# Performance work log

Hardware: AMD Instinct MI355X
Metric: run time of the kernel (lower is better)

The kernel has to match this reference:

```python
import jax, jax.numpy as jnp
import numpy as np

G1, G2, G3 = 4.0, 5.0, 10.0   # cfg.SMOOTH.GAMMA1/2/3 (DAMSM defaults)
T_MOCO = 0.05
EPS = 1e-8


def _ce(logits, labels):
    # mean cross-entropy, labels are int class indices
    lp = jax.nn.log_softmax(logits, axis=-1)
    return -jnp.mean(jnp.take_along_axis(lp, labels[:, None], axis=1)[:, 0])


def _norm(x):
    return jnp.sqrt(jnp.sum(x * x, axis=-1, keepdims=True))


def setup_inputs() -> dict:
    key = jax.random.key(0)
    ks = jax.random.split(key, 8)
    B, T, NEF, H, K = 64, 32, 256, 17, 16384
    return {
        "cnn_code": jax.random.normal(ks[0], (B, NEF), jnp.float32),
        "rnn_code": jax.random.normal(ks[1], (B, NEF), jnp.float32),
        "img_features": jax.random.normal(ks[2], (B, NEF, H, H), jnp.float32),
        "words_emb": jax.random.normal(ks[3], (B, T, NEF), jnp.float32),
        "cnn_code_aug": jax.random.normal(ks[4], (B, NEF), jnp.float32),
        "rnn_code_aug": jax.random.normal(ks[5], (B, NEF), jnp.float32),
        "queue": jax.random.normal(ks[6], (NEF, K), jnp.float32),
        "queue_im": jax.random.normal(ks[7], (NEF, K), jnp.float32),
        "sentence_mask": jnp.ones((B, T), jnp.int32),
        "labels": jnp.arange(B, dtype=jnp.int32),
    }


def reference(cnn_code, rnn_code, img_features, words_emb, cnn_code_aug,
              rnn_code_aug, queue, queue_im, sentence_mask, labels):
    B = words_emb.shape[0]
    # ---------- local word-region attention loss (vectorized over the
    # per-sample python loop; sentence_mask is all-ones -> full length) ----------
    q = jnp.transpose(words_emb, (0, 2, 1))                   # [B, nef, T]
    ctx = img_features.reshape(B, img_features.shape[1], -1)  # [B, nef, S]
    # func_attention: scores[i,j,s,t] between query sample i and image j
    scores = jnp.einsum('jcs,ict->ijst', ctx, q)
    attn = jax.nn.softmax(scores, axis=3)        # softmax over words (queryL)
    attn = jax.nn.softmax(G1 * attn, axis=2)     # softmax over regions (sourceL)
    wC = jnp.einsum('jcs,ijst->ijct', ctx, attn)  # weighted context [i,j,nef,T]
    num = jnp.einsum('ict,ijct->ijt', q, wC)
    qn = jnp.sqrt(jnp.sum(q * q, axis=1))[:, None, :]         # [B,1,T]
    wn = jnp.sqrt(jnp.sum(wC * wC, axis=2))                   # [B,B,T]
    cos = num / jnp.clip(qn * wn, EPS, None)                  # [i,j,T]
    sim = jax.nn.logsumexp(G2 * cos, axis=2)                  # log(sum exp(G2*cos))
    S = sim.T * G3                                            # [j, i] as in original cat(dim=1)
    w_loss0 = _ce(S, labels)
    w_loss1 = _ce(S.T, labels)
    # ---------- global contrastive loss ----------
    cn = cnn_code / jnp.clip(_norm(cnn_code), EPS, None)
    rn = rnn_code / jnp.clip(_norm(rnn_code), EPS, None)
    can = cnn_code_aug / jnp.clip(_norm(cnn_code_aug), EPS, None)
    ran = rnn_code_aug / jnp.clip(_norm(rnn_code_aug), EPS, None)
    qz = jax.lax.stop_gradient(queue)
    qzi = jax.lax.stop_gradient(queue_im)
    zeros = jnp.zeros((B,), dtype=labels.dtype)
    log_it = jnp.concatenate([jnp.sum(cn * ran, -1, keepdims=True), cn @ qz], -1) / T_MOCO
    log_ti = jnp.concatenate([jnp.sum(rn * can, -1, keepdims=True), rn @ qzi], -1) / T_MOCO
    m_loss = (_ce(log_it, zeros) + _ce(log_ti, zeros)) / 2.0
    s0 = G3 * (cn @ rn.T)    # cosine(cnn, rnn) * GAMMA3
    s2 = G3 * (rn @ ran.T)   # cosine(rnn, rnn_aug) * GAMMA3
    loss0 = _ce(s0, labels)
    loss1 = _ce(s0.T, labels)
    loss2 = _ce(s2, labels)
    loss3 = _ce(s2.T, labels)
    return jnp.stack([w_loss0, w_loss1, loss0, loss1, m_loss, loss2, loss3])
```

## Files before the change

### kernel.cpp

```cpp
#include <hip/hip_runtime.h>
#include <hip/hip_bf16.h>
#include <math.h>

#define BB   64
#define TT   32
#define CC   256
#define KK   16384
#define G1c  4.0f
#define G2c  5.0f
#define G3c  10.0f
#define INV_T 20.0f
#define EPSF 1e-8f

#define WS_SIM 0
#define WS_S0  4096
#define WS_S2  8192
#define WS_CN  12288
#define WS_RN  28672
#define WS_CAN 45056
#define WS_RAN 61440
#define WS_QN  77824
#define WS_PM  79872
#define WS_PS  (WS_PM + 16384)
#define WS_CNT  (WS_PS + 16384)
#define WS_RNT  (WS_CNT + 16384)
#define WS_CANT (WS_RNT + 16384)
#define WS_RANT (WS_CANT + 16384)
#define WS_F32_TOTAL (WS_RANT + 16384)

#define CTXT_ELEMS (64*320*256)
#define WQ_ELEMS   (64*32*256)
#define WQ_OFF     CTXT_ELEMS
#define CNRN_OFF   (CTXT_ELEMS + WQ_ELEMS)

typedef __attribute__((ext_vector_type(8))) short short8;
typedef __attribute__((ext_vector_type(4))) short short4v;
typedef __attribute__((ext_vector_type(4))) float float4v;

__device__ __forceinline__ float4v mfma_bf16(short8 a, short8 b, float4v c) {
    return __builtin_amdgcn_mfma_f32_16x16x32_bf16(a, b, c, 0, 0, 0);
}

__device__ __forceinline__ short f2bf(float f) {
    union { float f; unsigned u; } x; x.f = f;
    unsigned r = x.u + 0x7FFFu + ((x.u >> 16) & 1u);
    return (short)(r >> 16);
}

__device__ __forceinline__ int swz13(int L) {
    return L ^ (((L>>10)&3)<<4) ^ ((((L>>6)&1) ^ ((L>>10)&1))<<3);
}

__device__ __forceinline__ void stage_tile(const short* g, short* l) {
    #pragma unroll
    for (int m = 0; m < 4; m++)
        __builtin_amdgcn_global_load_lds(
            (const __attribute__((address_space(1))) unsigned int*)(g + m*512),
            (__attribute__((address_space(3))) unsigned int*)(l + m*512),
            16, 0, 0);
}

__global__ __launch_bounds__(256) void prep_kernel(
    const float* __restrict__ cnn, const float* __restrict__ rnn,
    const float* __restrict__ img, const float* __restrict__ wemb,
    const float* __restrict__ cnnA, const float* __restrict__ rnnA,
    float* __restrict__ W)
{
    int bid = blockIdx.x, tid = threadIdx.x;
    short* B16 = (short*)(W + WS_F32_TOTAL);
    short* ctxT = B16;
    short* wq   = B16 + WQ_OFF;
    short* cnrn = B16 + CNRN_OFF;

    if (bid < 256) {
        int mat = bid >> 6, row = bid & 63;
        const float* src = (mat==0)? cnn : (mat==1)? rnn : (mat==2)? cnnA : rnnA;
        float* dst  = W + ((mat==0)? WS_CN  : (mat==1)? WS_RN  : (mat==2)? WS_CAN  : WS_RAN);
        float* dstT = W + ((mat==0)? WS_CNT : (mat==1)? WS_RNT : (mat==2)? WS_CANT : WS_RANT);
        float v = src[row*256 + tid];
        float ss = v*v;
        for (int o=1;o<64;o<<=1) ss += __shfl_xor(ss,o);
        __shared__ float sc[4];
        if ((tid&63)==0) sc[tid>>6] = ss;
        __syncthreads();
        float tot = sc[0]+sc[1]+sc[2]+sc[3];
        float inv = 1.0f / fmaxf(sqrtf(tot), EPSF);
        float nv = v*inv;
        dst[row*256+tid] = nv;
        dstT[tid*64+row] = nv;
        if (mat < 2) cnrn[(mat*64+row)*256 + tid] = f2bf(nv);
    } else if (bid < 320) {
        int i = bid - 256;
        int t = tid >> 3, k = tid & 7;
        const float* wp = wemb + (i*32 + t)*256 + k*32;
        float ss = 0.f;
        for (int c=0;c<32;c++){ float v = wp[c]; ss += v*v; }
        ss += __shfl_xor(ss,1); ss += __shfl_xor(ss,2); ss += __shfl_xor(ss,4);
        if (k==0) W[WS_QN + i*32 + t] = sqrtf(ss);
    } else if (bid < 1600) {
        int b3 = bid - 320; int j = b3 / 20, mt20 = b3 % 20;
        int half = mt20 & 1;
        int s0 = mt20 * 16;
        __shared__ float tbuf[16*257];
        for (int idx = tid; idx < 4096; idx += 256) {
            int c = idx >> 4, sl = idx & 15, s = s0 + sl;
            float v = (s < 289) ? img[((size_t)(j*256 + c))*289 + s] : 0.0f;
            tbuf[sl*257 + c] = v;
        }
        __syncthreads();
        short* dst = ctxT + (size_t)j*81920 + (size_t)mt20*4096;
        for (int idx4 = tid; idx4 < 1024; idx4 += 256) {
            int v = half*4096 + idx4*4;
            int L = swz13(v);
            int sl = ((L>>10)&3)*4 + ((L>>4)&3);
            int c  = ((L>>6)&15)*16 + (L&15);
            const float* tb = &tbuf[sl*257 + c];
            short4v o = { f2bf(tb[0]), f2bf(tb[1]), f2bf(tb[2]), f2bf(tb[3]) };
            *(short4v*)(dst + idx4*4) = o;
        }
    } else {
        for (int idx = (bid-1600)*256 + tid; idx < WQ_ELEMS; idx += 64*256) {
            wq[idx] = f2bf(wemb[idx]);
        }
    }
}

__global__ __launch_bounds__(256, 2) void attn_moco_kernel(
    const float* __restrict__ queue, const float* __restrict__ queueIm,
    float* __restrict__ W)
{
    __shared__ __align__(16) short ctx_sc[2][8192];
    __shared__ __align__(16) short eTile[2][2][32][40];
    __shared__ float Dp[4][32], Np[4][32];
    __shared__ float wn2P[4][2][2][16];
    __shared__ float redm[4][64], reds[4][64];
    __shared__ float sa0[256], sa1[256];
    __shared__ float part[2][64][4];

    int bid = blockIdx.x, tid = threadIdx.x;
    int lane = tid & 63, wave = tid >> 6;
    int lo16 = lane & 15, quad = lane >> 4;

    const short* B16 = (const short*)(W + WS_F32_TOTAL);

    if (bid >= 320) {
        const short* ctxT = B16;
        const short* wq   = B16 + WQ_OFF;

        int abid = bid - 320;
        int j = abid >> 5, ip = abid & 31;
        int i_l = wave >> 1, mt = wave & 1;
        int i_g = ip*2 + i_l;

        short8 bq[2][8];
        {
            const short* p = wq + i_g*8192;
            #pragma unroll
            for (int nt2=0;nt2<2;nt2++)
                #pragma unroll
                for (int kk=0;kk<8;kk++)
                    bq[nt2][kk] = *(const short8*)(p + (nt2*16+lo16)*256 + kk*32 + quad*8);
        }

        float4v wacc[4][4];
        #pragma unroll
        for (int cm=0;cm<4;cm++)
            #pragma unroll
            for (int cb=0;cb<4;cb++) wacc[cm][cb] = (float4v){0.f,0.f,0.f,0.f};
        float D8[8], N8[8];
        #pragma unroll
        for (int u=0;u<8;u++){ D8[u]=0.f; N8[u]=0.f; }

        const short* ctxTj = ctxT + (size_t)j * 81920;

        int s4p = lo16 >> 2;
        int qh = quad >> 1, ql = quad & 1;
        int Lb = (mt*4 + s4p)*1024 + qh*64
               + (((lo16&3) ^ s4p) << 4)
               + ((ql ^ qh ^ (s4p&1)) << 3);
        int pcol = mt*16 + (lo16 & 12) + ((lo16 & 3) ^ s4p);
        unsigned trbase = (unsigned)(unsigned long long)(const void*)(&ctx_sc[0][0])
                        + (unsigned)(quad*4096 + wave*512 + lo16*2);

        stage_tile(ctxTj + 0*8192 + wave*2048 + lane*8, &ctx_sc[0][wave*2048]);
        stage_tile(ctxTj + 1*8192 + wave*2048 + lane*8, &ctx_sc[1][wave*2048]);
        __syncthreads();

        for (int tile = 0; tile < 10; tile++) {
            int cur = tile & 1;
            const short* score_base = &ctx_sc[cur][0] + Lb;

            float4v a0 = {0.f,0.f,0.f,0.f}, a1 = {0.f,0.f,0.f,0.f};
            #pragma unroll
            for (int kk=0;kk<8;kk++) {
                short8 cf = *(const short8*)(score_base + kk*128);
                a0 = mfma_bf16(bq[0][kk], cf, a0);
                a1 = mfma_bf16(bq[1][kk], cf, a1);
            }

            unsigned trA = trbase + (unsigned)(cur*16384);
            unsigned trB = trA ^ 16u;
            short4v w00,w01,w10,w11,w20,w21,w30,w31;
            asm volatile("ds_read_b64_tr_b16 %0, %1 offset:0"    : "=v"(w00) : "v"(trA));
            asm volatile("ds_read_b64_tr_b16 %0, %1 offset:2048" : "=v"(w01) : "v"(trB));
            asm volatile("ds_read_b64_tr_b16 %0, %1 offset:128"  : "=v"(w10) : "v"(trB));
            asm volatile("ds_read_b64_tr_b16 %0, %1 offset:2176" : "=v"(w11) : "v"(trA));
            asm volatile("ds_read_b64_tr_b16 %0, %1 offset:256"  : "=v"(w20) : "v"(trA));
            asm volatile("ds_read_b64_tr_b16 %0, %1 offset:2304" : "=v"(w21) : "v"(trB));
            asm volatile("ds_read_b64_tr_b16 %0, %1 offset:384"  : "=v"(w30) : "v"(trB));
            asm volatile("ds_read_b64_tr_b16 %0, %1 offset:2432" : "=v"(w31) : "v"(trA));

            float mx = fmaxf(fmaxf(fmaxf(a0[0],a0[1]), fmaxf(a0[2],a0[3])),
                             fmaxf(fmaxf(a1[0],a1[1]), fmaxf(a1[2],a1[3])));
            mx = fmaxf(mx, __shfl_xor(mx,16));
            mx = fmaxf(mx, __shfl_xor(mx,32));
            float e0[4], e1[4]; float z = 0.f;
            #pragma unroll
            for (int r=0;r<4;r++) {
                e0[r] = __expf(a0[r]-mx); e1[r] = __expf(a1[r]-mx);
                z += e0[r] + e1[r];
            }
            z += __shfl_xor(z,16); z += __shfl_xor(z,32);
            float grinv = G1c / z;
            int sg = tile*32 + mt*16 + lo16;
            short* et = &eTile[cur][i_l][0][0];
            #pragma unroll
            for (int r=0;r<4;r++) {
                float ev0 = __expf(e0[r]*grinv);
                float ev1 = __expf(e1[r]*grinv);
                if (sg < 289) {
                    D8[r]   += ev0; N8[r]   += ev0*a0[r];
                    D8[4+r] += ev1; N8[4+r] += ev1*a1[r];
                }
                et[(quad*4+r)*40 + pcol]    = f2bf(ev0);
                et[(16+quad*4+r)*40 + pcol] = f2bf(ev1);
            }
            __syncthreads();
            __builtin_amdgcn_sched_barrier(0);
            if (tile < 8)
                stage_tile(ctxTj + (tile+2)*8192 + wave*2048 + lane*8,
                           &ctx_sc[cur][wave*2048]);

            short8 wa_[4];
            wa_[0] = (short8){w00[0],w00[1],w00[2],w00[3], w01[0],w01[1],w01[2],w01[3]};
            wa_[1] = (short8){w10[0],w10[1],w10[2],w10[3], w11[0],w11[1],w11[2],w11[3]};
            wa_[2] = (short8){w20[0],w20[1],w20[2],w20[3], w21[0],w21[1],w21[2],w21[3]};
            wa_[3] = (short8){w30[0],w30[1],w30[2],w30[3], w31[0],w31[1],w31[2],w31[3]};
            {
                const short8 bf00 = *(const short8*)&eTile[cur][0][lo16][quad*8];
                const short8 bf01 = *(const short8*)&eTile[cur][0][16+lo16][quad*8];
                const short8 bf10 = *(const short8*)&eTile[cur][1][lo16][quad*8];
                const short8 bf11 = *(const short8*)&eTile[cur][1][16+lo16][quad*8];
                #pragma unroll
                for (int cm=0;cm<4;cm++) {
                    wacc[cm][0] = mfma_bf16(wa_[cm], bf00, wacc[cm][0]);
                    wacc[cm][1] = mfma_bf16(wa_[cm], bf01, wacc[cm][1]);
                    wacc[cm][2] = mfma_bf16(wa_[cm], bf10, wacc[cm][2]);
                    wacc[cm][3] = mfma_bf16(wa_[cm], bf11, wacc[cm][3]);
                }
            }
        }

        #pragma unroll
        for (int u=0;u<8;u++) {
            float d = D8[u], n = N8[u];
            d += __shfl_xor(d,1); d += __shfl_xor(d,2);
            d += __shfl_xor(d,4); d += __shfl_xor(d,8);
            n += __shfl_xor(n,1); n += __shfl_xor(n,2);
            n += __shfl_xor(n,4); n += __shfl_xor(n,8);
            if (lo16 == 0) {
                int t = (u>>2)*16 + quad*4 + (u&3);
                Dp[wave][t] = d; Np[wave][t] = n;
            }
        }
        #pragma unroll
        for (int cb=0;cb<4;cb++) {
            float ss = 0.f;
            #pragma unroll
            for (int cm=0;cm<4;cm++)
                #pragma unroll
                for (int r=0;r<4;r++){ float v = wacc[cm][cb][r]; ss += v*v; }
            ss += __shfl_xor(ss,16);
            ss += __shfl_xor(ss,32);
            if (quad==0) wn2P[wave][cb>>1][cb&1][lo16] = ss;
        }
        __syncthreads();

        if (tid < 64) {
            int i_f = tid >> 5, t = tid & 31;
            int nt2 = t >> 4, lo = t & 15;
            float w2 = wn2P[0][i_f][nt2][lo] + wn2P[1][i_f][nt2][lo]
                     + wn2P[2][i_f][nt2][lo] + wn2P[3][i_f][nt2][lo];
            float D = Dp[i_f*2][t] + Dp[i_f*2+1][t];
            float N = Np[i_f*2][t] + Np[i_f*2+1][t];
            int i_gf = ip*2 + i_f;
            float qv = W[WS_QN + i_gf*32 + t];
            float numS = N/D;
            float wnS = sqrtf(w2)/D;
            float v = G2c * (numS / fmaxf(qv*wnS, EPSF));
            float mx = v;
            for (int o=1;o<32;o<<=1) mx = fmaxf(mx, __shfl_xor(mx,o));
            float e = __expf(v-mx);
            for (int o=1;o<32;o<<=1) e += __shfl_xor(e,o);
            if (t==0) W[WS_SIM + i_gf*64 + j] = mx + __logf(e);
        }
    } else if (bid < 256) {
        int mu = bid >> 7, ch = bid & 127;
        const float* Q = mu ? queueIm : queue;
        const short* Abf = B16 + CNRN_OFF + mu*16384;

        short8 afr[4][8];
        #pragma unroll
        for (int mt=0;mt<4;mt++)
            #pragma unroll
            for (int kk=0;kk<8;kk++)
                afr[mt][kk] = *(const short8*)(Abf + (mt*16+lo16)*256 + kk*32 + quad*8);

        float m16[16], s16[16];
        #pragma unroll
        for (int u=0;u<16;u++){ m16[u] = -1e30f; s16[u] = 0.f; }

        for (int t4 = 0; t4 < 2; t4++) {
            int colb = ch*128 + (wave*2 + t4)*16;
            float4v acc[4];
            #pragma unroll
            for (int mt=0;mt<4;mt++) acc[mt] = (float4v){0.f,0.f,0.f,0.f};
            for (int ks = 0; ks < 8; ks++) {
                short8 bfr;
                #pragma unroll
                for (int jj=0;jj<8;jj++) {
                    float bv = Q[(size_t)(ks*32 + quad*8 + jj)*KK + colb + lo16];
                    bfr[jj] = f2bf(bv);
                }
                #pragma unroll
                for (int mt=0;mt<4;mt++) acc[mt] = mfma_bf16(afr[mt][ks], bfr, acc[mt]);
            }
            #pragma unroll
            for (int mt=0;mt<4;mt++)
                #pragma unroll
                for (int r=0;r<4;r++) {
                    float v = acc[mt][r]*INV_T;
                    int u = mt*4+r;
                    float nm = fmaxf(m16[u], v);
                    s16[u] = s16[u]*__expf(m16[u]-nm) + __expf(v-nm);
                    m16[u] = nm;
                }
        }
        #pragma unroll
        for (int u=0;u<16;u++) {
            #pragma unroll
            for (int o=1;o<16;o<<=1) {
                float om = __shfl_xor(m16[u],o), os = __shfl_xor(s16[u],o);
                float nm = fmaxf(m16[u],om);
                s16[u] = s16[u]*__expf(m16[u]-nm) + os*__expf(om-nm);
                m16[u] = nm;
            }
        }
        if (lo16 == 0) {
            #pragma unroll
            for (int u=0;u<16;u++) {
                int row = (u>>2)*16 + quad*4 + (u&3);
                redm[wave][row] = m16[u]; reds[wave][row] = s16[u];
            }
        }
        __syncthreads();
        if (tid < 64) {
            float m = redm[0][tid], s = reds[0][tid];
            for (int w=1;w<4;w++) {
                float om = redm[w][tid], os = reds[w][tid];
                float nm = fmaxf(m,om);
                s = s*__expf(m-nm) + os*__expf(om-nm);
                m = nm;
            }
            W[WS_PM + mu*8192 + ch*64 + tid] = m;
            W[WS_PS + mu*8192 + ch*64 + tid] = s;
        }
    } else {
        int i = bid - 256;
        sa0[tid] = W[WS_CN + i*256 + tid];
        sa1[tid] = W[WS_RN + i*256 + tid];
        __syncthreads();
        const float* B0 = W + WS_RN;
        const float* B1v = W + WS_RAN;
        float av0 = sa0[tid], av1 = sa1[tid];
        for (int jj = 0; jj < 64; jj++) {
            float v0 = av0 * B0[jj*256 + tid];
            float v1 = av1 * B1v[jj*256 + tid];
            for (int o=1;o<64;o<<=1){ v0 += __shfl_xor(v0,o); v1 += __shfl_xor(v1,o); }
            if (lane==0){ part[0][jj][wave]=v0; part[1][jj][wave]=v1; }
        }
        __syncthreads();
        if (tid < 128) {
            int mat = tid>>6, jj = tid&63;
            float s = part[mat][jj][0]+part[mat][jj][1]+part[mat][jj][2]+part[mat][jj][3];
            W[(mat? WS_S2 : WS_S0) + i*64 + jj] = G3c * s;
        }
    }
}

__global__ __launch_bounds__(256) void final_kernel(
    const int* __restrict__ labels, float* __restrict__ W, float* __restrict__ out)
{
    int tid = threadIdx.x;
    __shared__ float mats[3][64][65];
    __shared__ float mmL[2][4][64], ssL[2][4][64];
    __shared__ float cearr[6][64];
    __shared__ float cemoco[128];

    for (int idx = tid; idx < 3*4096; idx += 256) {
        int t = idx >> 12, rem = idx & 4095;
        const float* src = W + (t==0 ? WS_SIM : (t==1 ? WS_S0 : WS_S2));
        mats[t][rem>>6][rem&63] = src[rem];
    }

    {
        int g = tid >> 6, r = tid & 63;
        for (int mu=0; mu<2; mu++) {
            float m = -1e30f, s = 0.f;
            for (int k=0; k<32; k++) {
                int ch = g*32 + k;
                float om = W[WS_PM + mu*8192 + ch*64 + r];
                float os = W[WS_PS + mu*8192 + ch*64 + r];
                float nm = fmaxf(m, om);
                s = s*__expf(m-nm) + os*__expf(om-nm);
                m = nm;
            }
            mmL[mu][g][r] = m; ssL[mu][g][r] = s;
        }
    }
    __syncthreads();

    if (tid < 128) {
        int mu = tid>>6, r = tid&63;
        float m = mmL[mu][0][r], s = ssL[mu][0][r];
        for (int g=1; g<4; g++) {
            float om = mmL[mu][g][r], os = ssL[mu][g][r];
            float nm = fmaxf(m, om);
            s = s*__expf(m-nm) + os*__expf(om-nm);
            m = nm;
        }
        const float* AT = W + (mu ? WS_RNT : WS_CNT);
        const float* BT = W + (mu ? WS_CANT : WS_RANT);
        float dot = 0.f;
        for (int c=0; c<256; c++) dot += AT[c*64 + r]*BT[c*64 + r];
        float v0 = dot*INV_T;
        float nm = fmaxf(m, v0);
        float S = s*__expf(m-nm) + __expf(v0-nm);
        cemoco[tid] = nm + __logf(S) - v0;
    }

    for (int pass=0; pass<2; pass++) {
        int cfg = pass*4 + (tid>>6);
        int row = tid&63;
        if (cfg < 6) {
            int mi; float scale; int colMajor;
            if (cfg==0){ mi=0; scale=G3c; colMajor=1; }
            else if (cfg==1){ mi=0; scale=G3c; colMajor=0; }
            else if (cfg==2){ mi=1; scale=1.f; colMajor=0; }
            else if (cfg==3){ mi=1; scale=1.f; colMajor=1; }
            else if (cfg==4){ mi=2; scale=1.f; colMajor=0; }
            else            { mi=2; scale=1.f; colMajor=1; }
            float mx = -1e30f;
            for (int x=0;x<64;x++) {
                float v = (colMajor? mats[mi][x][row] : mats[mi][row][x])*scale;
                mx = fmaxf(mx, v);
            }
            float se = 0.f;
            for (int x=0;x<64;x++) {
                float v = (colMajor? mats[mi][x][row] : mats[mi][row][x])*scale;
                se += __expf(v-mx);
            }
            int lbl = labels[row];
            float diag = (colMajor? mats[mi][lbl][row] : mats[mi][row][lbl])*scale;
            cearr[cfg][row] = mx + __logf(se) - diag;
        }
    }
    __syncthreads();

    if (tid < 7) {
        float r;
        if (tid == 4) {
            float s0=0.f, s1=0.f;
            for (int k=0;k<64;k++){ s0 += cemoco[k]; s1 += cemoco[64+k]; }
            r = (s0/64.f + s1/64.f)*0.5f;
        } else {
            int cfg = (tid < 4) ? tid : tid - 1;
            float s = 0.f;
            for (int k=0;k<64;k++) s += cearr[cfg][k];
            r = s/64.f;
        }
        out[tid] = r;
    }
}

extern "C" void kernel_launch(void* const* d_in, const int* in_sizes, int n_in,
                              void* d_out, int out_size, void* d_ws, size_t ws_size,
                              hipStream_t stream)
{
    const float* cnn   = (const float*)d_in[0];
    const float* rnn   = (const float*)d_in[1];
    const float* img   = (const float*)d_in[2];
    const float* wemb  = (const float*)d_in[3];
    const float* cnnA  = (const float*)d_in[4];
    const float* rnnA  = (const float*)d_in[5];
    const float* queue   = (const float*)d_in[6];
    const float* queueIm = (const float*)d_in[7];
    const int*   labels  = (const int*)d_in[9];
    float* W   = (float*)d_ws;
    float* out = (float*)d_out;

    prep_kernel<<<1664, 256, 0, stream>>>(cnn, rnn, img, wemb, cnnA, rnnA, W);
    attn_moco_kernel<<<2368, 256, 0, stream>>>(queue, queueIm, W);
    final_kernel<<<1, 256, 0, stream>>>(labels, W, out);
}
```

Measured before the change: 226.4 us.

## Triple-buffer context tiles with partial vmcnt waits and remap block order

Grows the shared-memory context staging from two to three buffers so tile loads are issued three tiles ahead. The full __syncthreads is replaced with explicit s_waitcnt vmcnt/lgkmcnt plus s_barrier, so the barrier waits only for the oldest outstanding load. Block indices are also permuted so that consecutive blocks land on different j images, which changes how they spread across the chip and share L2. The extra 16KB of LDS per block may reduce occupancy below the 2-block launch bound, and the hand-counted vmcnt values depend on how many loads stage_tile issues.

```diff
diff --git a/kernel.cpp b/kernel.cpp
--- a/kernel.cpp
+++ b/kernel.cpp
@@ -129,7 +129,7 @@
     const float* __restrict__ queue, const float* __restrict__ queueIm,
     float* __restrict__ W)
 {
-    __shared__ __align__(16) short ctx_sc[2][8192];
+    __shared__ __align__(16) short ctx_sc[3][8192];
     __shared__ __align__(16) short eTile[2][2][32][40];
     __shared__ float Dp[4][32], Np[4][32];
     __shared__ float wn2P[4][2][2][16];
@@ -147,7 +147,8 @@
         const short* ctxT = B16;
         const short* wq   = B16 + WQ_OFF;
 
-        int abid = bid - 320;
+        int abid0 = bid - 320;
+        int abid = (abid0 & 7)*256 + (abid0 >> 3);
         int j = abid >> 5, ip = abid & 31;
         int i_l = wave >> 1, mt = wave & 1;
         int i_g = ip*2 + i_l;
@@ -184,11 +185,14 @@
 
         stage_tile(ctxTj + 0*8192 + wave*2048 + lane*8, &ctx_sc[0][wave*2048]);
         stage_tile(ctxTj + 1*8192 + wave*2048 + lane*8, &ctx_sc[1][wave*2048]);
-        __syncthreads();
-
+        stage_tile(ctxTj + 2*8192 + wave*2048 + lane*8, &ctx_sc[2][wave*2048]);
+        asm volatile("s_waitcnt vmcnt(8)\n\ts_barrier" ::: "memory");
+        __builtin_amdgcn_sched_barrier(0);
+
+        int cb3 = 0;
         for (int tile = 0; tile < 10; tile++) {
-            int cur = tile & 1;
-            const short* score_base = &ctx_sc[cur][0] + Lb;
+            int eb = tile & 1;
+            const short* score_base = &ctx_sc[cb3][0] + Lb;
 
             float4v a0 = {0.f,0.f,0.f,0.f}, a1 = {0.f,0.f,0.f,0.f};
             #pragma unroll
@@ -198,7 +202,7 @@
                 a1 = mfma_bf16(bq[1][kk], cf, a1);
             }
 
-            unsigned trA = trbase + (unsigned)(cur*16384);
+            unsigned trA = trbase + (unsigned)(cb3*16384);
             unsigned trB = trA ^ 16u;
             short4v w00,w01,w10,w11,w20,w21,w30,w31;
             asm volatile("ds_read_b64_tr_b16 %0, %1 offset:0"    : "=v"(w00) : "v"(trA));
@@ -223,7 +227,7 @@
             z += __shfl_xor(z,16); z += __shfl_xor(z,32);
             float grinv = G1c / z;
             int sg = tile*32 + mt*16 + lo16;
-            short* et = &eTile[cur][i_l][0][0];
+            short* et = &eTile[eb][i_l][0][0];
             #pragma unroll
             for (int r=0;r<4;r++) {
                 float ev0 = __expf(e0[r]*grinv);
@@ -235,11 +239,15 @@
                 et[(quad*4+r)*40 + pcol]    = f2bf(ev0);
                 et[(16+quad*4+r)*40 + pcol] = f2bf(ev1);
             }
-            __syncthreads();
+
+            if (tile < 8)
+                asm volatile("s_waitcnt lgkmcnt(0)\n\ts_waitcnt vmcnt(4)\n\ts_barrier" ::: "memory");
+            else
+                asm volatile("s_waitcnt lgkmcnt(0)\n\ts_waitcnt vmcnt(0)\n\ts_barrier" ::: "memory");
             __builtin_amdgcn_sched_barrier(0);
-            if (tile < 8)
-                stage_tile(ctxTj + (tile+2)*8192 + wave*2048 + lane*8,
-                           &ctx_sc[cur][wave*2048]);
+            if (tile < 7)
+                stage_tile(ctxTj + (tile+3)*8192 + wave*2048 + lane*8,
+                           &ctx_sc[cb3][wave*2048]);
 
             short8 wa_[4];
             wa_[0] = (short8){w00[0],w00[1],w00[2],w00[3], w01[0],w01[1],w01[2],w01[3]};
@@ -247,10 +255,10 @@
             wa_[2] = (short8){w20[0],w20[1],w20[2],w20[3], w21[0],w21[1],w21[2],w21[3]};
             wa_[3] = (short8){w30[0],w30[1],w30[2],w30[3], w31[0],w31[1],w31[2],w31[3]};
             {
-                const short8 bf00 = *(const short8*)&eTile[cur][0][lo16][quad*8];
-                const short8 bf01 = *(const short8*)&eTile[cur][0][16+lo16][quad*8];
-                const short8 bf10 = *(const short8*)&eTile[cur][1][lo16][quad*8];
-                const short8 bf11 = *(const short8*)&eTile[cur][1][16+lo16][quad*8];
+                const short8 bf00 = *(const short8*)&eTile[eb][0][lo16][quad*8];
+                const short8 bf01 = *(const short8*)&eTile[eb][0][16+lo16][quad*8];
+                const short8 bf10 = *(const short8*)&eTile[eb][1][lo16][quad*8];
+                const short8 bf11 = *(const short8*)&eTile[eb][1][16+lo16][quad*8];
                 #pragma unroll
                 for (int cm=0;cm<4;cm++) {
                     wacc[cm][0] = mfma_bf16(wa_[cm], bf00, wacc[cm][0]);
@@ -259,6 +267,7 @@
                     wacc[cm][3] = mfma_bf16(wa_[cm], bf11, wacc[cm][3]);
                 }
             }
+            cb3 = (cb3 == 2) ? 0 : cb3 + 1;
         }
 
         #pragma unroll
```

New measurement: 230.1 us. About the same (+1.6%).
